# Kernel tuning notes

Measured on AMD Instinct MI355X. Metric: run time of the kernel, lower is better.

The kernel has to match this reference:

```python
import jax, jax.numpy as jnp
import numpy as np

B, T, V, U = 16, 2048, 1024, 256
BLANK = 0
LOG_THR = float(np.log(3.0))  # spike_threshold = 3.0


def setup_inputs() -> dict:
    key = jax.random.key(0)
    k1, k2, k3, k4, k5 = jax.random.split(key, 5)
    alpha = jax.random.normal(k1, (B, T), dtype=jnp.float32)
    logits = jax.random.normal(k2, (B, T, V), dtype=jnp.float32)
    # boost blank logit per-frame so blank prob (and thus triggering) varies
    blank_boost = 3.0 * jax.random.normal(k3, (B, T), dtype=jnp.float32) + jnp.log(float(V))
    logits = logits.at[:, :, BLANK].add(blank_boost)
    ctc_log_probs = jax.nn.log_softmax(logits, axis=-1)
    frame_len = jax.random.randint(k4, (B,), T // 2, T + 1)
    mask = (jnp.arange(T)[None, :] < frame_len[:, None]).astype(jnp.float32)
    text_length = jax.random.randint(k5, (B,), 1, U + 1).astype(jnp.int64)
    return {"alpha": alpha, "ctc_log_probs": ctc_log_probs, "mask": mask,
            "text_length": text_length}


def reference(alpha, ctc_log_probs, mask, text_length):
    # Faithful to the torch module, including the `m <= end` quirk: since all
    # segment end indices are >= 1, the boolean mask compares (0/1) <= end and
    # is True everywhere, so every segment sum equals sum(alpha[i, :]).
    bsz = alpha.shape[0]
    blank_logp = ctc_log_probs[:, :, BLANK]                       # [B,T]
    triggered = (1.0 - blank_logp) > LOG_THR                      # [B,T] bool
    spikes = triggered.astype(mask.dtype) * mask                  # [B,T]
    # spikes row is prepended with a 1 at index 0 (begin); nonzero indices of
    # that row have sum > 0 iff there is at least one real spike.
    n_real = jnp.sum(spikes != 0, axis=1)                         # [B] int
    has_seg = n_real >= 1
    n_seg = n_real                                                # (1+n_real) spikes -> n_real segments
    row_sum = jnp.sum(alpha, axis=1)                              # [B]
    len_i = jnp.where(has_seg, n_seg, 1)                          # padded row lengths

    W = T + 1                                                     # static upper bound on boundary width
    j = jnp.arange(W)[None, :]                                    # [1,W]
    seg_cols = has_seg[:, None] & (j < n_seg[:, None])
    ones_col = (~has_seg)[:, None] & (j == 0)
    boundary = jnp.where(seg_cols, row_sum[:, None],
                         jnp.where(ones_col, 1.0, 0.0))           # [B,W]

    # torch truncates to min(max padded boundary width, max text length)
    L = jnp.minimum(jnp.max(len_i), jnp.max(text_length))
    text_mask = (j < text_length[:, None]) & (j < L)              # [B,W]
    per_sample = jnp.sum(jnp.abs(boundary - 1.0) * text_mask.astype(alpha.dtype), axis=1)
    return jnp.sum(per_sample) / bsz
```

## Files before the change

### kernel.cpp

```cpp
#include <hip/hip_runtime.h>

#define BB 16
#define TT 2048
#define VV 1024
#define LOG_THR 1.0986122886681098f

__global__ void ctc_stage1(const float* __restrict__ alpha,
                           const float* __restrict__ ctc,
                           const float* __restrict__ mask,
                           float* __restrict__ ws_sum,
                           int* __restrict__ ws_cnt) {
    const int b = blockIdx.x;
    const int tid = threadIdx.x;
    const float* arow = alpha + (size_t)b * TT;
    const float* mrow = mask + (size_t)b * TT;
    const float* crow = ctc + (size_t)b * TT * VV;

    float s = 0.0f;
    int c = 0;
    for (int t = tid; t < TT; t += blockDim.x) {
        s += arow[t];
        float lp = crow[(size_t)t * VV];
        float mk = mrow[t];
        if ((1.0f - lp) > LOG_THR && mk != 0.0f) c++;
    }

    for (int off = 32; off > 0; off >>= 1) {
        s += __shfl_down(s, off, 64);
        c += __shfl_down(c, off, 64);
    }

    __shared__ float ssum[8];
    __shared__ int   scnt[8];
    const int wave = tid >> 6;
    if ((tid & 63) == 0) { ssum[wave] = s; scnt[wave] = c; }
    __syncthreads();
    if (tid == 0) {
        float ts = 0.0f; int tc = 0;
        const int nw = blockDim.x >> 6;
        for (int w = 0; w < nw; ++w) { ts += ssum[w]; tc += scnt[w]; }
        ws_sum[b] = ts;
        ws_cnt[b] = tc;
    }
}

__global__ void ctc_stage2(const float* __restrict__ ws_sum,
                           const int* __restrict__ ws_cnt,
                           const int* __restrict__ text_length,
                           float* __restrict__ out) {
    const int lane = threadIdx.x;

    float rs = 0.0f;
    int cnt = 0, tl = 0;
    if (lane < BB) {
        rs  = ws_sum[lane];
        cnt = ws_cnt[lane];
        tl  = text_length[lane];
    }

    int len_i = (lane < BB) ? (cnt >= 1 ? cnt : 1) : 0;
    int tlv   = (lane < BB) ? tl : 0;

    int ml = len_i, mt = tlv;
    for (int off = 32; off > 0; off >>= 1) {
        ml = max(ml, __shfl_down(ml, off, 64));
        mt = max(mt, __shfl_down(mt, off, 64));
    }
    ml = __shfl(ml, 0, 64);
    mt = __shfl(mt, 0, 64);
    const int L = min(ml, mt);

    float per = 0.0f;
    if (lane < BB) {
        const int m = min(tl, L);
        if (cnt >= 1) {
            const int k = min(cnt, m);
            per = (float)k * fabsf(rs - 1.0f) + (float)max(0, m - cnt);
        } else {
            per = (float)max(0, m - 1);
        }
    }
    for (int off = 32; off > 0; off >>= 1) per += __shfl_down(per, off, 64);

    if (lane == 0) out[0] = per / (float)BB;
}

extern "C" void kernel_launch(void* const* d_in, const int* in_sizes, int n_in,
                              void* d_out, int out_size, void* d_ws, size_t ws_size,
                              hipStream_t stream) {
    const float* alpha       = (const float*)d_in[0];
    const float* ctc         = (const float*)d_in[1];
    const float* mask        = (const float*)d_in[2];
    const int*   text_length = (const int*)d_in[3];

    float* ws_sum = (float*)d_ws;
    int*   ws_cnt = (int*)((char*)d_ws + 256);
    float* out    = (float*)d_out;

    ctc_stage1<<<BB, 256, 0, stream>>>(alpha, ctc, mask, ws_sum, ws_cnt);
    ctc_stage2<<<1, 64, 0, stream>>>(ws_sum, ws_cnt, text_length, out);
}
```

Measured before the change: 172.8 us.

## Split per-row reduction across 16 chunk blocks per batch row

Stage 1 now launches one 128-thread block per (batch, time-chunk) pair, 256 blocks in total instead of 16. Each thread loads one frame, and the per-chunk partial sums and counts go to workspace. Stage 2 first reduces the 16 partials per row, then applies the same loss formula. The point is to spread the strided single-element gathers from the large log-prob tensor over many more CUs and raise memory-level parallelism, at the cost of a two-level reduction and more workspace.

Result: faster. 169.0 us (-2.2%).

```diff
diff --git a/kernel.cpp b/kernel.cpp
--- a/kernel.cpp
+++ b/kernel.cpp
@@ -3,86 +3,93 @@
 #define BB 16
 #define TT 2048
 #define VV 1024
+#define CH 16
+#define CT (TT / CH)
 #define LOG_THR 1.0986122886681098f
 
-__global__ void ctc_stage1(const float* __restrict__ alpha,
-                           const float* __restrict__ ctc,
-                           const float* __restrict__ mask,
-                           float* __restrict__ ws_sum,
-                           int* __restrict__ ws_cnt) {
-    const int b = blockIdx.x;
+__global__ __launch_bounds__(CT) void ctc_stage1(
+        const float* __restrict__ alpha,
+        const float* __restrict__ ctc,
+        const float* __restrict__ mask,
+        float* __restrict__ ws_sum,
+        int* __restrict__ ws_cnt) {
+    const int b   = blockIdx.x >> 4;
+    const int ch  = blockIdx.x & 15;
     const int tid = threadIdx.x;
-    const float* arow = alpha + (size_t)b * TT;
-    const float* mrow = mask + (size_t)b * TT;
-    const float* crow = ctc + (size_t)b * TT * VV;
+    const int t   = ch * CT + tid;
 
-    float s = 0.0f;
-    int c = 0;
-    for (int t = tid; t < TT; t += blockDim.x) {
-        s += arow[t];
-        float lp = crow[(size_t)t * VV];
-        float mk = mrow[t];
-        if ((1.0f - lp) > LOG_THR && mk != 0.0f) c++;
+    const size_t idx = (size_t)b * TT + t;
+    float s  = alpha[idx];
+    float mk = mask[idx];
+    float lp = ctc[idx * (size_t)VV];
+    int   c  = ((1.0f - lp) > LOG_THR && mk != 0.0f) ? 1 : 0;
+
+    #pragma unroll
+    for (int off = 32; off > 0; off >>= 1) {
+        s += __shfl_xor(s, off, 64);
+        c += __shfl_xor(c, off, 64);
     }
 
-    for (int off = 32; off > 0; off >>= 1) {
-        s += __shfl_down(s, off, 64);
-        c += __shfl_down(c, off, 64);
-    }
-
-    __shared__ float ssum[8];
-    __shared__ int   scnt[8];
-    const int wave = tid >> 6;
-    if ((tid & 63) == 0) { ssum[wave] = s; scnt[wave] = c; }
+    __shared__ float ssum[CT / 64];
+    __shared__ int   scnt[CT / 64];
+    if ((tid & 63) == 0) { ssum[tid >> 6] = s; scnt[tid >> 6] = c; }
     __syncthreads();
     if (tid == 0) {
         float ts = 0.0f; int tc = 0;
-        const int nw = blockDim.x >> 6;
-        for (int w = 0; w < nw; ++w) { ts += ssum[w]; tc += scnt[w]; }
-        ws_sum[b] = ts;
-        ws_cnt[b] = tc;
+        #pragma unroll
+        for (int w = 0; w < CT / 64; ++w) { ts += ssum[w]; tc += scnt[w]; }
+        ws_sum[b * CH + ch] = ts;
+        ws_cnt[b * CH + ch] = tc;
     }
 }
 
-__global__ void ctc_stage2(const float* __restrict__ ws_sum,
-                           const int* __restrict__ ws_cnt,
-                           const int* __restrict__ text_length,
-                           float* __restrict__ out) {
-    const int lane = threadIdx.x;
+__global__ __launch_bounds__(256) void ctc_stage2(
+        const float* __restrict__ ws_sum,
+        const int* __restrict__ ws_cnt,
+        const int* __restrict__ text_length,
+        float* __restrict__ out) {
+    const int tid = threadIdx.x;
 
-    float rs = 0.0f;
-    int cnt = 0, tl = 0;
-    if (lane < BB) {
-        rs  = ws_sum[lane];
-        cnt = ws_cnt[lane];
-        tl  = text_length[lane];
+    float s = ws_sum[tid];
+    int   c = ws_cnt[tid];
+    #pragma unroll
+    for (int off = 8; off > 0; off >>= 1) {
+        s += __shfl_xor(s, off, 64);
+        c += __shfl_xor(c, off, 64);
     }
 
-    int len_i = (lane < BB) ? (cnt >= 1 ? cnt : 1) : 0;
-    int tlv   = (lane < BB) ? tl : 0;
+    __shared__ float rs_sh[BB];
+    __shared__ int   cnt_sh[BB];
+    if ((tid & 15) == 0) { rs_sh[tid >> 4] = s; cnt_sh[tid >> 4] = c; }
+    __syncthreads();
 
-    int ml = len_i, mt = tlv;
-    for (int off = 32; off > 0; off >>= 1) {
-        ml = max(ml, __shfl_down(ml, off, 64));
-        mt = max(mt, __shfl_down(mt, off, 64));
-    }
-    ml = __shfl(ml, 0, 64);
-    mt = __shfl(mt, 0, 64);
-    const int L = min(ml, mt);
+    if (tid < BB) {
+        const float rs  = rs_sh[tid];
+        const int   cnt = cnt_sh[tid];
+        const int   tl  = text_length[tid];
 
-    float per = 0.0f;
-    if (lane < BB) {
+        int len_i = (cnt >= 1) ? cnt : 1;
+        int ml = len_i, mt = tl;
+        #pragma unroll
+        for (int off = 8; off > 0; off >>= 1) {
+            ml = max(ml, __shfl_xor(ml, off, 64));
+            mt = max(mt, __shfl_xor(mt, off, 64));
+        }
+        const int L = min(ml, mt);
         const int m = min(tl, L);
+
+        float per;
         if (cnt >= 1) {
             const int k = min(cnt, m);
             per = (float)k * fabsf(rs - 1.0f) + (float)max(0, m - cnt);
         } else {
             per = (float)max(0, m - 1);
         }
+        #pragma unroll
+        for (int off = 8; off > 0; off >>= 1) per += __shfl_xor(per, off, 64);
+
+        if (tid == 0) out[0] = per / (float)BB;
     }
-    for (int off = 32; off > 0; off >>= 1) per += __shfl_down(per, off, 64);
-
-    if (lane == 0) out[0] = per / (float)BB;
 }
 
 extern "C" void kernel_launch(void* const* d_in, const int* in_sizes, int n_in,
@@ -94,9 +101,9 @@
     const int*   text_length = (const int*)d_in[3];
 
     float* ws_sum = (float*)d_ws;
-    int*   ws_cnt = (int*)((char*)d_ws + 256);
+    int*   ws_cnt = (int*)((char*)d_ws + 1024);
     float* out    = (float*)d_out;
 
-    ctc_stage1<<<BB, 256, 0, stream>>>(alpha, ctc, mask, ws_sum, ws_cnt);
-    ctc_stage2<<<1, 64, 0, stream>>>(ws_sum, ws_cnt, text_length, out);
+    ctc_stage1<<<BB * CH, CT, 0, stream>>>(alpha, ctc, mask, ws_sum, ws_cnt);
+    ctc_stage2<<<1, 256, 0, stream>>>(ws_sum, ws_cnt, text_length, out);
 }
```
